# Performance work log

Measured on AMD Instinct MI355X. Metric: run time of the kernel, lower is better.

## Reference

```python
import jax, jax.numpy as jnp
import numpy as np


def setup_inputs() -> dict:
    key = jax.random.key(0)
    k1, k2, k3, k4 = jax.random.split(key, 4)
    b, c_in, t, h, w = 8, 64, 16, 64, 64
    c_out, kh, kw = 64, 3, 3
    x = jax.random.normal(k1, (b, c_in, t, h, w), dtype=jnp.float32)
    alpha = jax.random.uniform(k2, (b, c_in, t, 1, 1), dtype=jnp.float32)
    fan_in = c_in * kh * kw
    weight = jax.random.normal(k3, (c_out, c_in, kh, kw), dtype=jnp.float32) / np.sqrt(fan_in)
    bias = jax.random.normal(k4, (c_out,), dtype=jnp.float32) * 0.05
    return {"x": x, "alpha": alpha, "weight": weight, "bias": bias}


def reference(x, alpha, weight, bias):
    # x: (b, c_in, t, h, w); alpha: (b, c_in, t, 1, 1)
    # weight: (c_out, c_in, kh, kw); bias: (c_out,)
    b, c_in, t, h, w = x.shape
    c_out, _, kh, kw = weight.shape
    pad = ((kh // 2, kh // 2), (kw // 2, kw // 2))  # padding=1 for 3x3
    # per-(b,t) calibrated weights: alpha scales the c_in dim (cal_dim='cin')
    a = jnp.transpose(alpha[..., 0, 0], (0, 2, 1))          # (b, t, c_in)
    w_bt = a[:, :, None, :, None, None] * weight[None, None]  # (b, t, c_out, c_in, kh, kw)
    xs = jnp.transpose(x, (0, 2, 1, 3, 4)).reshape(b * t, 1, c_in, h, w)
    ws = w_bt.reshape(b * t, c_out, c_in, kh, kw)

    def conv_one(xi, wi):
        return jax.lax.conv_general_dilated(
            xi, wi, window_strides=(1, 1), padding=pad,
            dimension_numbers=("NCHW", "OIHW", "NCHW"))[0]

    out = jax.vmap(conv_one)(xs, ws)                          # (b*t, c_out, h, w)
    out = out + bias[None, :, None, None]
    out = out.reshape(b, t, c_out, h, w).transpose(0, 2, 1, 3, 4)
    return out  # (b, c_out, t, h, w)
```

## Files before the change

### kernel.cpp

```cpp
#include <hip/hip_runtime.h>


#define CIN  64
#define COUT 64
#define TT   16
#define BB   8
#define HH   64
#define WW   64

typedef __attribute__((ext_vector_type(8))) short bf16x8;
typedef __attribute__((ext_vector_type(4))) float f32x4;

__device__ __forceinline__ unsigned short f2bf(float f) {
    union { float f; unsigned u; } v; v.f = f;
    unsigned r = (v.u + 0x7FFF + ((v.u >> 16) & 1)) >> 16;
    return (unsigned short)r;
}

__global__ __launch_bounds__(256) void prep_x(const float* __restrict__ x,
                                              const float* __restrict__ alpha,
                                              int4* __restrict__ xh) {
    __shared__ float ls[64 * 66];
    const int blk = blockIdx.x;
    const int h   = blk & 63;
    const int bt  = blk >> 6;
    const int t   = bt & 15;
    const int b   = bt >> 4;
    const int tid = threadIdx.x;

#pragma unroll
    for (int it = 0; it < 4; ++it) {
        int idx4 = tid + it * 256;
        int ci   = idx4 >> 4;
        int w4   = (idx4 & 15) * 4;
        float a  = alpha[(b * CIN + ci) * TT + t];
        const float* gp = x + (((b * CIN + ci) * TT + t) * HH + h) * WW + w4;
        float4 v = *(const float4*)gp;
        ls[(w4 + 0) * 66 + ci] = v.x * a;
        ls[(w4 + 1) * 66 + ci] = v.y * a;
        ls[(w4 + 2) * 66 + ci] = v.z * a;
        ls[(w4 + 3) * 66 + ci] = v.w * a;
    }
    __syncthreads();

#pragma unroll
    for (int it = 0; it < 2; ++it) {
        int tau  = tid + it * 256;
        int w    = tau >> 3;
        int slot = tau & 7;
        int g    = slot ^ (w & 7);
        const float* p = &ls[w * 66 + g * 8];
        float2 p0 = *(const float2*)(p + 0);
        float2 p1 = *(const float2*)(p + 2);
        float2 p2 = *(const float2*)(p + 4);
        float2 p3 = *(const float2*)(p + 6);
        int4 o;
        o.x = (int)f2bf(p0.x) | ((int)f2bf(p0.y) << 16);
        o.y = (int)f2bf(p1.x) | ((int)f2bf(p1.y) << 16);
        o.z = (int)f2bf(p2.x) | ((int)f2bf(p2.y) << 16);
        o.w = (int)f2bf(p3.x) | ((int)f2bf(p3.y) << 16);
        xh[((bt * 64 + h) * 64 + w) * 8 + slot] = o;
    }
}

__global__ __launch_bounds__(256) void prep_w(const float* __restrict__ wgt,
                                              unsigned short* __restrict__ wb) {
    int idx = blockIdx.x * 256 + threadIdx.x;
    if (idx < COUT * CIN * 9) {
        int co  = idx / (CIN * 9);
        int r   = idx - co * (CIN * 9);
        int ci  = r / 9;
        int tap = r - ci * 9;
        int slot = (ci >> 3) ^ (co & 7);
        wb[((tap * COUT + co) * 8 + slot) * 8 + (ci & 7)] = f2bf(wgt[idx]);
    }
}

__global__ __launch_bounds__(256) void conv2(const short* __restrict__ xh,
                                             const short* __restrict__ wb,
                                             const float* __restrict__ bias,
                                             float* __restrict__ out) {
    __shared__ __align__(16) short xs[4][66 * 64];
    __shared__ __align__(16) short wl[2][64 * 64];

    const int blk   = blockIdx.x;
    const int ytile = blk & 31;
    const int bt    = blk >> 5;
    const int t     = bt & 15;
    const int b     = bt >> 4;
    const int y0    = ytile * 2;
    const int tid   = threadIdx.x;
    const int wave  = tid >> 6;
    const int lane  = tid & 63;

    {
        const int r  = wave;
        const int gy = y0 - 1 + r;
        int4* dst = (int4*)xs[r];
        if ((unsigned)gy < HH) {
            const int4* src = (const int4*)(xh + (bt * 64 + gy) * 64 * 64);
            int4* d = (int4*)(xs[r] + 64);
#pragma unroll
            for (int it = 0; it < 8; ++it) d[it * 64 + lane] = src[it * 64 + lane];
            int4 z = {0, 0, 0, 0};
            if (lane < 8)       dst[lane] = z;
            else if (lane < 16) ((int4*)(xs[r] + 4160))[lane - 8] = z;
        } else {
            int4 z = {0, 0, 0, 0};
#pragma unroll
            for (int it = 0; it < 9; ++it) {
                int idx = it * 64 + lane;
                if (idx < 528) dst[idx] = z;
            }
        }
    }
    {
        const int4* src = (const int4*)wb;
        int4* d = (int4*)wl[0];
        d[tid] = src[tid];
        d[tid + 256] = src[tid + 256];
    }
    __syncthreads();

    f32x4 acc[4][2] = {};
    const int ywave = wave >> 1;
    const int wseg  = (wave & 1) * 32;
    const int co_l  = lane & 15;
    const int kg    = lane >> 4;

    for (int tap = 0; tap < 9; ++tap) {
        const int cur = tap & 1;
        int4 wp0, wp1;
        if (tap < 8) {
            const int4* src = (const int4*)(wb + (tap + 1) * 4096);
            wp0 = src[tid];
            wp1 = src[tid + 256];
        }
        const int ky = tap / 3;
        const int dx = (tap - 3 * ky) - 1;
        const short* xrow = xs[ywave + ky];
        const short* wcur = wl[cur];

#pragma unroll
        for (int kc = 0; kc < 2; ++kc) {
            const int g = kc * 4 + kg;
            bf16x8 af[4];
#pragma unroll
            for (int m = 0; m < 4; ++m) {
                int co   = m * 16 + co_l;
                int slot = g ^ (co & 7);
                af[m] = *(const bf16x8*)(wcur + co * 64 + slot * 8);
            }
            bf16x8 bfr[2];
#pragma unroll
            for (int nt = 0; nt < 2; ++nt) {
                int w    = wseg + nt * 16 + co_l;
                int wx   = w + dx;
                int slot = g ^ (wx & 7);
                bfr[nt] = *(const bf16x8*)(xrow + (wx + 1) * 64 + slot * 8);
            }
#pragma unroll
            for (int m = 0; m < 4; ++m)
#pragma unroll
                for (int nt = 0; nt < 2; ++nt)
                    acc[m][nt] = __builtin_amdgcn_mfma_f32_16x16x32_bf16(
                        af[m], bfr[nt], acc[m][nt], 0, 0, 0);
        }

        if (tap < 8) {
            int4* d = (int4*)wl[cur ^ 1];
            d[tid] = wp0;
            d[tid + 256] = wp1;
        }
        __syncthreads();
    }

    const int y = y0 + ywave;
#pragma unroll
    for (int m = 0; m < 4; ++m) {
#pragma unroll
        for (int r = 0; r < 4; ++r) {
            int co = m * 16 + (lane >> 4) * 4 + r;
            float bv = bias[co];
            float* op = out + (((b * COUT + co) * TT + t) * HH + y) * WW;
#pragma unroll
            for (int nt = 0; nt < 2; ++nt) {
                int w = wseg + nt * 16 + co_l;
                op[w] = acc[m][nt][r] + bv;
            }
        }
    }
}

extern "C" void kernel_launch(void* const* d_in, const int* in_sizes, int n_in,
                              void* d_out, int out_size, void* d_ws, size_t ws_size,
                              hipStream_t stream) {
    const float* x      = (const float*)d_in[0];
    const float* alpha  = (const float*)d_in[1];
    const float* weight = (const float*)d_in[2];
    const float* bias   = (const float*)d_in[3];
    float* out          = (float*)d_out;

    unsigned short* wb = (unsigned short*)d_ws;
    short* xhat = (short*)((char*)d_ws + (128 << 10));

    hipLaunchKernelGGL(prep_w, dim3(144), dim3(256), 0, stream, weight, wb);
    hipLaunchKernelGGL(prep_x, dim3(BB * TT * HH), dim3(256), 0, stream,
                       x, alpha, (int4*)xhat);
    hipLaunchKernelGGL(conv2, dim3(BB * TT * (HH / 2)), dim3(256), 0, stream,
                       xhat, (const short*)wb, bias, out);
}
```

Before: 285.6 us.

## Fuse alpha scaling and bf16 conversion into conv kernel, enlarge row tile

Removes the separate prep_x kernel and its intermediate bf16 buffer. The conv kernel now reads fp32 x directly, scales it by alpha, converts to bf16 into swizzled LDS, and computes four output rows per block with 512 threads. Block indices are remapped to spread neighbouring tiles across XCDs. This drops a full write and read of the intermediate activation tensor. In exchange the conv kernel carries the conversion work, uses more LDS per block, and each block now re-reads two halo rows across four output rows rather than two.

Result: faster. 261.2 us (-8.5%).

```diff
diff --git a/kernel.cpp b/kernel.cpp
--- a/kernel.cpp
+++ b/kernel.cpp
@@ -17,52 +17,6 @@
     return (unsigned short)r;
 }
 
-__global__ __launch_bounds__(256) void prep_x(const float* __restrict__ x,
-                                              const float* __restrict__ alpha,
-                                              int4* __restrict__ xh) {
-    __shared__ float ls[64 * 66];
-    const int blk = blockIdx.x;
-    const int h   = blk & 63;
-    const int bt  = blk >> 6;
-    const int t   = bt & 15;
-    const int b   = bt >> 4;
-    const int tid = threadIdx.x;
-
-#pragma unroll
-    for (int it = 0; it < 4; ++it) {
-        int idx4 = tid + it * 256;
-        int ci   = idx4 >> 4;
-        int w4   = (idx4 & 15) * 4;
-        float a  = alpha[(b * CIN + ci) * TT + t];
-        const float* gp = x + (((b * CIN + ci) * TT + t) * HH + h) * WW + w4;
-        float4 v = *(const float4*)gp;
-        ls[(w4 + 0) * 66 + ci] = v.x * a;
-        ls[(w4 + 1) * 66 + ci] = v.y * a;
-        ls[(w4 + 2) * 66 + ci] = v.z * a;
-        ls[(w4 + 3) * 66 + ci] = v.w * a;
-    }
-    __syncthreads();
-
-#pragma unroll
-    for (int it = 0; it < 2; ++it) {
-        int tau  = tid + it * 256;
-        int w    = tau >> 3;
-        int slot = tau & 7;
-        int g    = slot ^ (w & 7);
-        const float* p = &ls[w * 66 + g * 8];
-        float2 p0 = *(const float2*)(p + 0);
-        float2 p1 = *(const float2*)(p + 2);
-        float2 p2 = *(const float2*)(p + 4);
-        float2 p3 = *(const float2*)(p + 6);
-        int4 o;
-        o.x = (int)f2bf(p0.x) | ((int)f2bf(p0.y) << 16);
-        o.y = (int)f2bf(p1.x) | ((int)f2bf(p1.y) << 16);
-        o.z = (int)f2bf(p2.x) | ((int)f2bf(p2.y) << 16);
-        o.w = (int)f2bf(p3.x) | ((int)f2bf(p3.y) << 16);
-        xh[((bt * 64 + h) * 64 + w) * 8 + slot] = o;
-    }
-}
-
 __global__ __launch_bounds__(256) void prep_w(const float* __restrict__ wgt,
                                               unsigned short* __restrict__ wb) {
     int idx = blockIdx.x * 256 + threadIdx.x;
@@ -76,66 +30,78 @@
     }
 }
 
-__global__ __launch_bounds__(256) void conv2(const short* __restrict__ xh,
-                                             const short* __restrict__ wb,
-                                             const float* __restrict__ bias,
-                                             float* __restrict__ out) {
-    __shared__ __align__(16) short xs[4][66 * 64];
+__global__ __launch_bounds__(512, 4) void conv3(const float* __restrict__ x,
+                                                const float* __restrict__ alpha,
+                                                const short* __restrict__ wb,
+                                                const float* __restrict__ bias,
+                                                float* __restrict__ out) {
+    __shared__ __align__(16) short xs[6][66 * 64];
     __shared__ __align__(16) short wl[2][64 * 64];
 
-    const int blk   = blockIdx.x;
-    const int ytile = blk & 31;
-    const int bt    = blk >> 5;
+    const int orig  = blockIdx.x;
+    const int blk   = (orig & 7) * 256 + (orig >> 3);
+    const int ytile = blk & 15;
+    const int bt    = blk >> 4;
     const int t     = bt & 15;
     const int b     = bt >> 4;
-    const int y0    = ytile * 2;
+    const int y0    = ytile * 4;
     const int tid   = threadIdx.x;
-    const int wave  = tid >> 6;
+    const int wv    = tid >> 6;
     const int lane  = tid & 63;
 
     {
-        const int r  = wave;
-        const int gy = y0 - 1 + r;
-        int4* dst = (int4*)xs[r];
-        if ((unsigned)gy < HH) {
-            const int4* src = (const int4*)(xh + (bt * 64 + gy) * 64 * 64);
-            int4* d = (int4*)(xs[r] + 64);
+        const int cib = wv * 8;
+        float a0 = alpha[(b * CIN + cib + 0) * TT + t];
+        float a1 = alpha[(b * CIN + cib + 1) * TT + t];
+        float a2 = alpha[(b * CIN + cib + 2) * TT + t];
+        float a3 = alpha[(b * CIN + cib + 3) * TT + t];
+        float a4 = alpha[(b * CIN + cib + 4) * TT + t];
+        float a5 = alpha[(b * CIN + cib + 5) * TT + t];
+        float a6 = alpha[(b * CIN + cib + 6) * TT + t];
+        float a7 = alpha[(b * CIN + cib + 7) * TT + t];
+        const float* xb = x + (size_t)((b * CIN + cib) * TT + t) * (HH * WW);
+        const int slot = wv ^ (lane & 7);
+        const int CI_STRIDE = TT * HH * WW;
 #pragma unroll
-            for (int it = 0; it < 8; ++it) d[it * 64 + lane] = src[it * 64 + lane];
-            int4 z = {0, 0, 0, 0};
-            if (lane < 8)       dst[lane] = z;
-            else if (lane < 16) ((int4*)(xs[r] + 4160))[lane - 8] = z;
-        } else {
-            int4 z = {0, 0, 0, 0};
-#pragma unroll
-            for (int it = 0; it < 9; ++it) {
-                int idx = it * 64 + lane;
-                if (idx < 528) dst[idx] = z;
+        for (int r = 0; r < 6; ++r) {
+            const int gy = y0 - 1 + r;
+            int4 o = {0, 0, 0, 0};
+            if ((unsigned)gy < HH) {
+                const float* p = xb + gy * WW + lane;
+                float v0 = p[0 * CI_STRIDE] * a0;
+                float v1 = p[1 * CI_STRIDE] * a1;
+                float v2 = p[2 * CI_STRIDE] * a2;
+                float v3 = p[3 * CI_STRIDE] * a3;
+                float v4 = p[4 * CI_STRIDE] * a4;
+                float v5 = p[5 * CI_STRIDE] * a5;
+                float v6 = p[6 * CI_STRIDE] * a6;
+                float v7 = p[7 * CI_STRIDE] * a7;
+                o.x = (int)f2bf(v0) | ((int)f2bf(v1) << 16);
+                o.y = (int)f2bf(v2) | ((int)f2bf(v3) << 16);
+                o.z = (int)f2bf(v4) | ((int)f2bf(v5) << 16);
+                o.w = (int)f2bf(v6) | ((int)f2bf(v7) << 16);
+            }
+            *(int4*)(xs[r] + (lane + 1) * 64 + slot * 8) = o;
+            if (lane < 2) {
+                int4 z = {0, 0, 0, 0};
+                *(int4*)(xs[r] + lane * 65 * 64 + wv * 8) = z;
             }
         }
     }
-    {
-        const int4* src = (const int4*)wb;
-        int4* d = (int4*)wl[0];
-        d[tid] = src[tid];
-        d[tid + 256] = src[tid + 256];
-    }
+    ((int4*)wl[0])[tid] = ((const int4*)wb)[tid];
     __syncthreads();
 
     f32x4 acc[4][2] = {};
-    const int ywave = wave >> 1;
-    const int wseg  = (wave & 1) * 32;
+    const int ywave = wv >> 1;
+    const int wseg  = (wv & 1) * 32;
     const int co_l  = lane & 15;
     const int kg    = lane >> 4;
 
     for (int tap = 0; tap < 9; ++tap) {
         const int cur = tap & 1;
-        int4 wp0, wp1;
-        if (tap < 8) {
-            const int4* src = (const int4*)(wb + (tap + 1) * 4096);
-            wp0 = src[tid];
-            wp1 = src[tid + 256];
-        }
+        int4 wp;
+        if (tap < 8)
+            wp = ((const int4*)(wb + (tap + 1) * 4096))[tid];
         const int ky = tap / 3;
         const int dx = (tap - 3 * ky) - 1;
         const short* xrow = xs[ywave + ky];
@@ -167,11 +133,8 @@
                         af[m], bfr[nt], acc[m][nt], 0, 0, 0);
         }
 
-        if (tap < 8) {
-            int4* d = (int4*)wl[cur ^ 1];
-            d[tid] = wp0;
-            d[tid + 256] = wp1;
-        }
+        if (tap < 8)
+            ((int4*)wl[cur ^ 1])[tid] = wp;
         __syncthreads();
     }
 
@@ -180,9 +143,9 @@
     for (int m = 0; m < 4; ++m) {
 #pragma unroll
         for (int r = 0; r < 4; ++r) {
-            int co = m * 16 + (lane >> 4) * 4 + r;
+            int co = m * 16 + kg * 4 + r;
             float bv = bias[co];
-            float* op = out + (((b * COUT + co) * TT + t) * HH + y) * WW;
+            float* op = out + (size_t)(((b * COUT + co) * TT + t) * HH + y) * WW;
 #pragma unroll
             for (int nt = 0; nt < 2; ++nt) {
                 int w = wseg + nt * 16 + co_l;
@@ -202,11 +165,8 @@
     float* out          = (float*)d_out;
 
     unsigned short* wb = (unsigned short*)d_ws;
-    short* xhat = (short*)((char*)d_ws + (128 << 10));
 
     hipLaunchKernelGGL(prep_w, dim3(144), dim3(256), 0, stream, weight, wb);
-    hipLaunchKernelGGL(prep_x, dim3(BB * TT * HH), dim3(256), 0, stream,
-                       x, alpha, (int4*)xhat);
-    hipLaunchKernelGGL(conv2, dim3(BB * TT * (HH / 2)), dim3(256), 0, stream,
-                       xhat, (const short*)wb, bias, out);
+    hipLaunchKernelGGL(conv3, dim3(BB * TT * (HH / 4)), dim3(512), 0, stream,
+                       x, alpha, (const short*)wb, bias, out);
 }
```
